# Kernel optimization log

Measured on AMD Instinct MI355X. Metric: run time of the kernel, lower is better.

## Reference

```python
import jax, jax.numpy as jnp
import numpy as np
from jax import lax

DILS = (1, 2, 4, 8)
POOLS = (1, 2, 3, 6)
EPS = 1e-3  # Keras BatchNormalization default epsilon


def conv2d(x, w, b, dil=1):
    y = lax.conv_general_dilated(x, w, window_strides=(1, 1), padding='SAME',
                                 rhs_dilation=(dil, dil),
                                 dimension_numbers=('NHWC', 'HWIO', 'NHWC'))
    return y + b


def bn(x, g, be, m, v):
    return (x - m) * (g * lax.rsqrt(v + EPS)) + be


def avg_pool_same(x, ps):
    if ps == 1:
        return x
    win = (1, ps, ps, 1)
    s = lax.reduce_window(x, 0.0, lax.add, win, win, 'SAME')
    c = lax.reduce_window(jnp.ones(x.shape[:3] + (1,), x.dtype), 0.0, lax.add, win, win, 'SAME')
    return s / c  # TF avg-pool SAME excludes padded zeros from the count


def setup_inputs() -> dict:
    key = jax.random.key(0)
    ks = iter(jax.random.split(key, 40))
    f = 64  # filters
    cin = 64
    d = {}
    d['x'] = jax.random.normal(next(ks), (2, 64, 64, cin), jnp.float32)
    nb = len(DILS)
    d['conv_w'] = jax.random.normal(next(ks), (nb, 3, 3, cin, f)) * 0.05
    d['conv_b'] = jax.random.normal(next(ks), (nb, f)) * 0.05
    d['bn_g'] = jnp.ones((nb, f)) + jax.random.normal(next(ks), (nb, f)) * 0.05
    d['bn_b'] = jax.random.normal(next(ks), (nb, f)) * 0.05
    d['bn_m'] = jax.random.normal(next(ks), (nb, f)) * 0.05
    d['bn_v'] = jax.random.uniform(next(ks), (nb, f), minval=0.5, maxval=1.5)
    dk = f // 8
    d['q_w'] = jax.random.normal(next(ks), (nb, 1, 1, f, dk)) * 0.05
    d['q_b'] = jax.random.normal(next(ks), (nb, dk)) * 0.05
    d['k_w'] = jax.random.normal(next(ks), (nb, 1, 1, f, dk)) * 0.05
    d['k_b'] = jax.random.normal(next(ks), (nb, dk)) * 0.05
    d['v_w'] = jax.random.normal(next(ks), (nb, 1, 1, f, f)) * 0.05
    d['v_b'] = jax.random.normal(next(ks), (nb, f)) * 0.05
    d['attn_gamma'] = jax.random.normal(next(ks), (nb,)) * 0.1
    cat = f * nb  # 256, input channels to pyramid convs
    npool = len(POOLS)
    fq = f // 4  # 16
    d['ppl_w'] = jax.random.normal(next(ks), (npool, 1, 1, cat, fq)) * 0.05
    d['ppl_b'] = jax.random.normal(next(ks), (npool, fq)) * 0.05
    d['ppl_bn_g'] = jnp.ones((npool, fq)) + jax.random.normal(next(ks), (npool, fq)) * 0.05
    d['ppl_bn_b'] = jax.random.normal(next(ks), (npool, fq)) * 0.05
    d['ppl_bn_m'] = jax.random.normal(next(ks), (npool, fq)) * 0.05
    d['ppl_bn_v'] = jax.random.uniform(next(ks), (npool, fq), minval=0.5, maxval=1.5)
    cfused = cat + npool * fq  # 320
    d['proj_w'] = jax.random.normal(next(ks), (1, 1, cfused, f)) * 0.05
    d['proj_b'] = jax.random.normal(next(ks), (f,)) * 0.05
    d['pbn_g'] = jnp.ones((f,)) + jax.random.normal(next(ks), (f,)) * 0.05
    d['pbn_b'] = jax.random.normal(next(ks), (f,)) * 0.05
    d['pbn_m'] = jax.random.normal(next(ks), (f,)) * 0.05
    d['pbn_v'] = jax.random.uniform(next(ks), (f,), minval=0.5, maxval=1.5)
    return d


def reference(x, conv_w, conv_b, bn_g, bn_b, bn_m, bn_v,
              q_w, q_b, k_w, k_b, v_w, v_b, attn_gamma,
              ppl_w, ppl_b, ppl_bn_g, ppl_bn_b, ppl_bn_m, ppl_bn_v,
              proj_w, proj_b, pbn_g, pbn_b, pbn_m, pbn_v):
    B, H, W, _ = x.shape
    branches = []
    for i, dil in enumerate(DILS):
        # dilated conv -> BN (inference) -> ReLU
        b = jax.nn.relu(bn(conv2d(x, conv_w[i], conv_b[i], dil),
                           bn_g[i], bn_b[i], bn_m[i], bn_v[i]))
        C = b.shape[-1]
        # full spatial self-attention over HW tokens
        q = conv2d(b, q_w[i], q_b[i]).reshape(B, H * W, -1)  # [B, HW, C/8]
        k = conv2d(b, k_w[i], k_b[i]).reshape(B, H * W, -1)
        v = conv2d(b, v_w[i], v_b[i]).reshape(B, H * W, C)
        attn = jax.nn.softmax(jnp.einsum('bnd,bmd->bnm', q, k), axis=-1)  # [B, HW, HW]
        o = jnp.einsum('bnm,bmc->bnc', attn, v).reshape(B, H, W, C)
        branches.append(attn_gamma[i] * o + b)
    fused = jnp.concatenate(branches, axis=-1)  # [B, H, W, 256]
    pooled = [fused]
    for j, ps in enumerate(POOLS):
        p = avg_pool_same(fused, ps)
        p = bn(conv2d(p, ppl_w[j], ppl_b[j]),
               ppl_bn_g[j], ppl_bn_b[j], ppl_bn_m[j], ppl_bn_v[j])
        p = jax.image.resize(p, (B, H, W, p.shape[-1]), method='bilinear')
        pooled.append(p)
    fused = jnp.concatenate(pooled, axis=-1)  # [B, H, W, 320]
    out = jax.nn.relu(bn(conv2d(fused, proj_w, proj_b), pbn_g, pbn_b, pbn_m, pbn_v))
    return out
```

## Files before the change

### kernel.cpp

```cpp
#include <hip/hip_runtime.h>
#include <hip/hip_bf16.h>
#include <stdint.h>

typedef unsigned short u16;
typedef short bs8 __attribute__((ext_vector_type(8)));
typedef unsigned short u16x4 __attribute__((ext_vector_type(4)));
typedef float vf4 __attribute__((ext_vector_type(4)));
typedef float vf16 __attribute__((ext_vector_type(16)));

__device__ __forceinline__ u16 f2bf(float f) {
    uint32_t u = __builtin_bit_cast(uint32_t, f);
    uint32_t r = u + 0x7FFFu + ((u >> 16) & 1u);
    return (u16)(r >> 16);
}
__device__ __forceinline__ float bf2f(u16 v) {
    return __builtin_bit_cast(float, (uint32_t)v << 16);
}

#define EPSBN 1e-3f
#define L2E 1.4426950408889634f

__global__ __launch_bounds__(256) void prep_k(
    const float* __restrict__ x, const float* __restrict__ cw,
    const float* __restrict__ qw, const float* __restrict__ kw,
    const float* __restrict__ vw, const float* __restrict__ pjw,
    u16* __restrict__ xbf, u16* __restrict__ wpk,
    u16* __restrict__ wqk_pk, u16* __restrict__ wv_pk, u16* __restrict__ wfin_pk)
{
    if (blockIdx.x < 512) {
        int t = blockIdx.x * 256 + threadIdx.x;
        int idx = t * 4;
        vf4 v = *(const vf4*)(x + idx);
        u16x4 o = { f2bf(v[0]), f2bf(v[1]), f2bf(v[2]), f2bf(v[3]) };
        *(u16x4*)(xbf + idx) = o;
    } else if (blockIdx.x < 1088) {
        int t2 = (blockIdx.x - 512) * 256 + threadIdx.x;
        if (t2 < 147456) {
            int cout = t2 & 63, rest = t2 >> 6;
            int cin = rest & 63, itap = rest >> 6;
            wpk[(((size_t)itap * 8 + (cin >> 3)) * 64 + cout) * 8 + (cin & 7)] = f2bf(cw[t2]);
        }
    } else if (blockIdx.x < 1168) {
        int t3 = (blockIdx.x - 1088) * 256 + threadIdx.x;
        if (t3 < 4096) {
            int j = t3 & 7, l = (t3 >> 3) & 63, kk = (t3 >> 9) & 1, i = t3 >> 10;
            int cin = kk * 32 + ((l >> 4) << 3) + j, row = l & 15;
            float val = (row < 8) ? qw[((size_t)(i * 64 + cin)) * 8 + row] * L2E
                                  : kw[((size_t)(i * 64 + cin)) * 8 + row - 8];
            wqk_pk[t3] = f2bf(val);
        } else {
            int e = t3 - 4096;
            int j = e & 7, l = (e >> 3) & 63, kk = (e >> 9) & 1;
            int ct = (e >> 10) & 3, i = e >> 12;
            int cin = kk * 32 + ((l >> 4) << 3) + j, cout = ct * 16 + (l & 15);
            wv_pk[e] = f2bf(vw[((size_t)(i * 64 + cin)) * 64 + cout]);
        }
    } else {
        int t4 = (blockIdx.x - 1168) * 256 + threadIdx.x;
        if (t4 < 20480) {
            int e = t4;
            int j = e & 7; e >>= 3;
            int rcol = e & 15; e >>= 4;
            int ct = e & 3; e >>= 2;
            int g = e & 3; int kc = e >> 2;
            int cin = kc * 32 + g * 8 + j, co = ct * 16 + rcol;
            wfin_pk[t4] = f2bf(pjw[(size_t)cin * 64 + co]);
        }
    }
}

__global__ __launch_bounds__(256) void conv_mfma_k(
    const u16* __restrict__ xbf, const u16* __restrict__ wpk,
    const float* __restrict__ cb, const float* __restrict__ bng,
    const float* __restrict__ bnb, const float* __restrict__ bnm,
    const float* __restrict__ bnv, const u16* __restrict__ wqk_pk,
    const u16* __restrict__ wv_pk, const float* __restrict__ qb,
    const float* __restrict__ kb, const float* __restrict__ vb,
    u16* __restrict__ b_bf, u16* __restrict__ qbuf,
    u16* __restrict__ kbuf, u16* __restrict__ vT)
{
    __shared__ u16 blds[32][72];
    const int ib = blockIdx.x & 7, pixtile = blockIdx.x >> 3;
    const int i = ib >> 1, b = ib & 1, dil = 1 << i;
    const int wave = __builtin_amdgcn_readfirstlane(threadIdx.x >> 6);
    const int lane = threadIdx.x & 63;
    const int g = lane >> 4, r = lane & 15;
    const int pixsub = wave & 1, ch = wave >> 1;
    const int pixbase = pixtile * 32 + pixsub * 16;
    const int h = pixbase >> 6, w0 = pixbase & 63;

    vf4 acc0 = {0.f, 0.f, 0.f, 0.f}, acc1 = {0.f, 0.f, 0.f, 0.f};

    for (int ky = 0; ky < 3; ++ky) {
        int hy = h + (ky - 1) * dil;
        if (hy < 0 || hy >= 64) continue;
        const u16* xrow = xbf + (size_t)((b * 64 + hy) * 64) * 64;
        for (int kx = 0; kx < 3; ++kx) {
            int wx = w0 + r + (kx - 1) * dil;
            bool valid = (wx >= 0) && (wx < 64);
            const u16* ap = xrow + (valid ? wx : 0) * 64 + g * 8;
            int tap = ky * 3 + kx;
            const u16* wb = wpk + (size_t)((i * 9 + tap) * 8) * 512;
#pragma unroll
            for (int c2 = 0; c2 < 2; ++c2) {
                bs8 av = {};
                if (valid) av = *(const bs8*)(ap + c2 * 32);
                const u16* bp = wb + (size_t)(c2 * 4 + g) * 512 + (ch * 32 + r) * 8;
                bs8 bv0 = *(const bs8*)(bp);
                bs8 bv1 = *(const bs8*)(bp + 16 * 8);
                acc0 = __builtin_amdgcn_mfma_f32_16x16x32_bf16(av, bv0, acc0, 0, 0, 0);
                acc1 = __builtin_amdgcn_mfma_f32_16x16x32_bf16(av, bv1, acc1, 0, 0, 0);
            }
        }
    }
#pragma unroll
    for (int ct = 0; ct < 2; ++ct) {
        int cidx = ch * 32 + ct * 16 + r;
        int cgl = i * 64 + cidx;
        float sc = bng[cgl] * rsqrtf(bnv[cgl] + EPSBN);
        float sh = (cb[cgl] - bnm[cgl]) * sc + bnb[cgl];
        vf4 a = ct ? acc1 : acc0;
#pragma unroll
        for (int rr = 0; rr < 4; ++rr) {
            float y = fmaxf(a[rr] * sc + sh, 0.f);
            u16 yb = f2bf(y);
            b_bf[((size_t)ib * 4096 + pixbase + g * 4 + rr) * 64 + cidx] = yb;
            blds[pixsub * 16 + g * 4 + rr][cidx] = yb;
        }
    }
    __syncthreads();

    const int ps2 = wave & 1, role = wave >> 1;
    const int n0 = pixtile * 32 + ps2 * 16;
    bs8 xb0 = *(const bs8*)(&blds[ps2 * 16 + r][g * 8]);
    bs8 xb1 = *(const bs8*)(&blds[ps2 * 16 + r][32 + g * 8]);

    if (role == 1) {
        const u16* wq = wqk_pk + (size_t)i * 1024 + lane * 8;
        bs8 wq0 = *(const bs8*)(wq);
        bs8 wq1 = *(const bs8*)(wq + 512);
        vf4 s = (vf4){0.f, 0.f, 0.f, 0.f};
        s = __builtin_amdgcn_mfma_f32_16x16x32_bf16(wq0, xb0, s, 0, 0, 0);
        s = __builtin_amdgcn_mfma_f32_16x16x32_bf16(wq1, xb1, s, 0, 0, 0);
        if (g < 2) {
            int d0 = g * 4;
            u16x4 o;
#pragma unroll
            for (int reg = 0; reg < 4; ++reg)
                o[reg] = f2bf(s[reg] + qb[i * 8 + d0 + reg] * L2E);
            *(u16x4*)(qbuf + ((size_t)ib * 4096 + n0 + r) * 8 + d0) = o;
        } else {
            int d0 = (g - 2) * 4;
            u16x4 o;
#pragma unroll
            for (int reg = 0; reg < 4; ++reg)
                o[reg] = f2bf(s[reg] + kb[i * 8 + d0 + reg]);
            *(u16x4*)(kbuf + ((size_t)ib * 4096 + n0 + r) * 8 + d0) = o;
        }
    }
#pragma unroll
    for (int c2t = 0; c2t < 2; ++c2t) {
        int ct = role * 2 + c2t;
        const u16* wv = wv_pk + ((size_t)i * 4 + ct) * 1024 + lane * 8;
        bs8 wv0 = *(const bs8*)(wv);
        bs8 wv1 = *(const bs8*)(wv + 512);
        vf4 a = (vf4){0.f, 0.f, 0.f, 0.f};
        a = __builtin_amdgcn_mfma_f32_16x16x32_bf16(wv0, xb0, a, 0, 0, 0);
        a = __builtin_amdgcn_mfma_f32_16x16x32_bf16(wv1, xb1, a, 0, 0, 0);
#pragma unroll
        for (int reg = 0; reg < 4; ++reg) {
            int row = ct * 16 + g * 4 + reg;
            vT[((size_t)ib * 64 + row) * 4096 + n0 + r] = f2bf(a[reg] + vb[i * 64 + row]);
        }
    }
}

__global__ __launch_bounds__(256) void attn_k(
    const u16* __restrict__ qbuf, const u16* __restrict__ kbuf,
    const u16* __restrict__ vT, u16* __restrict__ pacc,
    float* __restrict__ ppsum)
{
    __shared__ __align__(16) char smem[73728];

    const int bid = blockIdx.x;
    const int ib = bid & 7, ks = (bid >> 3) & 3, qblk = bid >> 5;
    const int yb = ks * 8 + ib;
    const int wave = __builtin_amdgcn_readfirstlane(threadIdx.x >> 6);
    const int lane = threadIdx.x & 63;
    const int ql = lane & 31;
    const int hb = lane >> 5;
    const int q0 = qblk * 256 + wave * 64;
    const int tid = threadIdx.x;

    const int kb_tbl[8] = {0, 8, 4, 12, 16, 24, 20, 28};
    const int kperm = (ql & 3) + kb_tbl[ql >> 2];

    bs8 qfa = {}, qfb = {};
    if (hb == 0) {
        qfa = *(const bs8*)(qbuf + ((size_t)ib * 4096 + q0 + ql) * 8);
        qfb = *(const bs8*)(qbuf + ((size_t)ib * 4096 + q0 + 32 + ql) * 8);
    }
    bs8 ones;
#pragma unroll
    for (int j = 0; j < 8; ++j) ones[j] = (short)0x3F80;

    vf16 a0a, a1a, a0b, a1b, sa, sb;
#pragma unroll
    for (int r = 0; r < 16; ++r) {
        a0a[r] = 0.f; a1a[r] = 0.f; a0b[r] = 0.f; a1b[r] = 0.f;
        sa[r] = 0.f; sb[r] = 0.f;
    }

    const u16* vsrc = vT + (size_t)ib * 64 * 4096;
    const u16* ksrc = kbuf + (size_t)ib * 4096 * 8;
    const int sc_ = tid >> 2, sp_ = tid & 3;

    bs8 vr[8]; bs8 kr;
    {
        const u16* vrow = vsrc + (size_t)sc_ * 4096 + (ks * 4) * 256;
#pragma unroll
        for (int s = 0; s < 8; ++s)
            vr[s] = *(const bs8*)(vrow + sp_ * 8 + s * 32);
        kr = *(const bs8*)(ksrc + (size_t)((ks * 4) * 256 + tid) * 8);
        char* ldsw = smem;
#pragma unroll
        for (int s = 0; s < 8; ++s) {
            int key = sp_ * 8 + s * 32;
            int lin = sc_ * 512 + key * 2;
            *(bs8*)(ldsw + (lin ^ ((sc_ & 7) << 4))) = vr[s];
        }
        *(bs8*)(ldsw + 32768 + tid * 16) = kr;
    }
    __syncthreads();

    for (int t = 0; t < 4; ++t) {
        if (t < 3) {
            const u16* vrow = vsrc + (size_t)sc_ * 4096 + (ks * 4 + t + 1) * 256;
#pragma unroll
            for (int s = 0; s < 8; ++s)
                vr[s] = *(const bs8*)(vrow + sp_ * 8 + s * 32);
            kr = *(const bs8*)(ksrc + (size_t)((ks * 4 + t + 1) * 256 + tid) * 8);
        }
        const char* ldsb = smem + (t & 1) * 36864;
        const u16* klds = (const u16*)(ldsb + 32768);

#pragma unroll 2
        for (int ck = 0; ck < 8; ++ck) {
            const int keyb = ck * 32;
            bs8 kA = {};
            if (hb == 0) kA = *(const bs8*)(klds + (keyb + kperm) * 8);
            vf16 z;
#pragma unroll
            for (int r = 0; r < 16; ++r) z[r] = 0.f;
            vf16 Sa = __builtin_amdgcn_mfma_f32_32x32x16_bf16(kA, qfa, z, 0, 0, 0);
            vf16 Sb = __builtin_amdgcn_mfma_f32_32x32x16_bf16(kA, qfb, z, 0, 0, 0);

            const int c0 = ql, c1 = 32 + ql;
            int lin00 = c0 * 512 + (keyb + hb * 8) * 2;
            int lin10 = c1 * 512 + (keyb + hb * 8) * 2;
            bs8 vA00 = *(const bs8*)(ldsb + (lin00 ^ ((c0 & 7) << 4)));
            bs8 vA01 = *(const bs8*)(ldsb + ((lin00 + 32) ^ ((c0 & 7) << 4)));
            bs8 vA10 = *(const bs8*)(ldsb + (lin10 ^ ((c1 & 7) << 4)));
            bs8 vA11 = *(const bs8*)(ldsb + ((lin10 + 32) ^ ((c1 & 7) << 4)));

            {
                float e[16];
#pragma unroll
                for (int r = 0; r < 16; ++r) e[r] = __builtin_amdgcn_exp2f(Sa[r]);
                union { uint32_t u[4]; bs8 v; } p0, p1;
#pragma unroll
                for (int j = 0; j < 4; ++j) {
                    uint32_t w0, w1;
                    asm("v_cvt_pk_bf16_f32 %0, %1, %2" : "=v"(w0) : "v"(e[2 * j]), "v"(e[2 * j + 1]));
                    asm("v_cvt_pk_bf16_f32 %0, %1, %2" : "=v"(w1) : "v"(e[8 + 2 * j]), "v"(e[8 + 2 * j + 1]));
                    p0.u[j] = w0;
                    p1.u[j] = w1;
                }
                sa = __builtin_amdgcn_mfma_f32_32x32x16_bf16(ones, p0.v, sa, 0, 0, 0);
                sa = __builtin_amdgcn_mfma_f32_32x32x16_bf16(ones, p1.v, sa, 0, 0, 0);
                a0a = __builtin_amdgcn_mfma_f32_32x32x16_bf16(vA00, p0.v, a0a, 0, 0, 0);
                a0a = __builtin_amdgcn_mfma_f32_32x32x16_bf16(vA01, p1.v, a0a, 0, 0, 0);
                a1a = __builtin_amdgcn_mfma_f32_32x32x16_bf16(vA10, p0.v, a1a, 0, 0, 0);
                a1a = __builtin_amdgcn_mfma_f32_32x32x16_bf16(vA11, p1.v, a1a, 0, 0, 0);
            }
            {
                float e[16];
#pragma unroll
                for (int r = 0; r < 16; ++r) e[r] = __builtin_amdgcn_exp2f(Sb[r]);
                union { uint32_t u[4]; bs8 v; } p0, p1;
#pragma unroll
                for (int j = 0; j < 4; ++j) {
                    uint32_t w0, w1;
                    asm("v_cvt_pk_bf16_f32 %0, %1, %2" : "=v"(w0) : "v"(e[2 * j]), "v"(e[2 * j + 1]));
                    asm("v_cvt_pk_bf16_f32 %0, %1, %2" : "=v"(w1) : "v"(e[8 + 2 * j]), "v"(e[8 + 2 * j + 1]));
                    p0.u[j] = w0;
                    p1.u[j] = w1;
                }
                sb = __builtin_amdgcn_mfma_f32_32x32x16_bf16(ones, p0.v, sb, 0, 0, 0);
                sb = __builtin_amdgcn_mfma_f32_32x32x16_bf16(ones, p1.v, sb, 0, 0, 0);
                a0b = __builtin_amdgcn_mfma_f32_32x32x16_bf16(vA00, p0.v, a0b, 0, 0, 0);
                a0b = __builtin_amdgcn_mfma_f32_32x32x16_bf16(vA01, p1.v, a0b, 0, 0, 0);
                a1b = __builtin_amdgcn_mfma_f32_32x32x16_bf16(vA10, p0.v, a1b, 0, 0, 0);
                a1b = __builtin_amdgcn_mfma_f32_32x32x16_bf16(vA11, p1.v, a1b, 0, 0, 0);
            }
        }

        if (t < 3) {
            char* ldsw = smem + ((t + 1) & 1) * 36864;
#pragma unroll
            for (int s = 0; s < 8; ++s) {
                int key = sp_ * 8 + s * 32;
                int lin = sc_ * 512 + key * 2;
                *(bs8*)(ldsw + (lin ^ ((sc_ & 7) << 4))) = vr[s];
            }
            *(bs8*)(ldsw + 32768 + tid * 16) = kr;
        }
        __syncthreads();
    }

    float* tw = (float*)smem + wave * 32 * 67;
#pragma unroll
    for (int t = 0; t < 2; ++t) {
        const int q0t = q0 + t * 32;
#pragma unroll
        for (int ct = 0; ct < 2; ++ct) {
            vf16 a = t ? (ct ? a1b : a0b) : (ct ? a1a : a0a);
#pragma unroll
            for (int r = 0; r < 16; ++r) {
                int c = ct * 32 + (r & 3) + 8 * (r >> 2) + 4 * hb;
                tw[ql * 67 + c] = a[r];
            }
        }
        __syncthreads();
        u16* pdst = pacc + ((size_t)yb * 4096 + q0t) * 64;
        for (int qq = 0; qq < 32; ++qq)
            pdst[(size_t)qq * 64 + lane] = f2bf(tw[qq * 67 + lane]);
        if (hb == 0)
            ppsum[(size_t)yb * 4096 + q0t + ql] = t ? sb[0] : sa[0];
    }
}

__global__ __launch_bounds__(256) void combine_k(
    const u16* __restrict__ pacc, const float* __restrict__ ppsum,
    const u16* __restrict__ b_bf, const float* __restrict__ gamma,
    u16* __restrict__ fusedbf)
{
    const int ib = blockIdx.x & 7, qb = blockIdx.x >> 3;
    const int i = ib >> 1, b = ib & 1;
    const int q = qb * 8 + (threadIdx.x >> 5);
    const int c2 = (threadIdx.x & 31) * 2;
    const size_t stride = (size_t)8 * 4096 * 64;
    size_t base = ((size_t)ib * 4096 + q) * 64 + c2;
    float lo = 0.f, hi = 0.f, ps = 0.f;
#pragma unroll
    for (int s = 0; s < 4; ++s) {
        uint32_t u = *(const uint32_t*)(pacc + base + s * stride);
        lo += bf2f((u16)(u & 0xffff));
        hi += bf2f((u16)(u >> 16));
        ps += ppsum[(size_t)(s * 8 + ib) * 4096 + q];
    }
    float rs = gamma[i] / ps;
    uint32_t bv = *(const uint32_t*)(b_bf + base);
    float o0 = rs * lo + bf2f((u16)(bv & 0xffff));
    float o1 = rs * hi + bf2f((u16)(bv >> 16));
    uint32_t ou = ((uint32_t)f2bf(o1) << 16) | f2bf(o0);
    *(uint32_t*)(fusedbf + ((size_t)b * 4096 + q) * 256 + i * 64 + c2) = ou;
}

__global__ __launch_bounds__(256) void pconv_k(
    const u16* __restrict__ fusedbf,
    const float* __restrict__ pw, const float* __restrict__ pbias,
    const float* __restrict__ pg, const float* __restrict__ pbe,
    const float* __restrict__ pm, const float* __restrict__ pv,
    float* __restrict__ po0, float* __restrict__ po1,
    float* __restrict__ po2, float* __restrict__ po3)
{
    __shared__ float plds[16][257];
    const int j = blockIdx.z, b = blockIdx.y;
    const int npix = (j == 0) ? 4096 : (j == 1) ? 1024 : (j == 2) ? 484 : 121;
    if (blockIdx.x * 16 >= npix) return;
    const int co = threadIdx.x & 15;
    const int pixl = threadIdx.x >> 4;
    const int pix = blockIdx.x * 16 + pixl;
    const float* wp = pw + (size_t)j * 256 * 16 + co;
    float acc = pbias[j * 16 + co];

    if (j == 0) {
        const u16* ip = fusedbf + ((size_t)b * 4096 + pix) * 256;
        for (int c8 = 0; c8 < 32; ++c8) {
            bs8 xv = *(const bs8*)(ip + c8 * 8);
#pragma unroll
            for (int e = 0; e < 8; ++e)
                acc = fmaf(bf2f((u16)xv[e]), wp[(c8 * 8 + e) * 16], acc);
        }
    } else {
        const int ps = (j == 1) ? 2 : (j == 2) ? 3 : 6;
        const int od = (j == 1) ? 32 : (j == 2) ? 22 : 11;
        if (pix < npix) {
            const int oh = pix / od, ow = pix % od;
            const int pad = (od * ps - 64) >> 1;
            int hs = oh * ps - pad, wss = ow * ps - pad;
            int h0 = max(hs, 0), h1 = min(hs + ps, 64);
            int w0 = max(wss, 0), w1 = min(wss + ps, 64);
            float s[16];
#pragma unroll
            for (int e = 0; e < 16; ++e) s[e] = 0.f;
            for (int hh = h0; hh < h1; ++hh)
                for (int ww = w0; ww < w1; ++ww) {
                    const u16* p = fusedbf + (((size_t)b * 4096) + hh * 64 + ww) * 256 + co * 16;
                    bs8 v0 = *(const bs8*)(p);
                    bs8 v1 = *(const bs8*)(p + 8);
#pragma unroll
                    for (int e = 0; e < 8; ++e) {
                        s[e] += bf2f((u16)v0[e]);
                        s[8 + e] += bf2f((u16)v1[e]);
                    }
                }
            float inv = 1.f / (float)((h1 - h0) * (w1 - w0));
#pragma unroll
            for (int e = 0; e < 16; ++e) plds[pixl][co * 16 + e] = s[e] * inv;
        }
        __syncthreads();
        if (pix < npix)
            for (int c = 0; c < 256; ++c)
                acc = fmaf(plds[pixl][c], wp[c * 16], acc);
    }
    if (pix < npix) {
        acc = (acc - pm[j * 16 + co]) * (pg[j * 16 + co] * rsqrtf(pv[j * 16 + co] + EPSBN)) + pbe[j * 16 + co];
        float* outp = (j == 0) ? po0 : (j == 1) ? po1 : (j == 2) ? po2 : po3;
        outp[((size_t)b * npix + pix) * 16 + co] = acc;
    }
}

__global__ __launch_bounds__(64) void final_gemm_k(
    const u16* __restrict__ fusedbf, const float* __restrict__ po0,
    const float* __restrict__ po1, const float* __restrict__ po2,
    const float* __restrict__ po3, const u16* __restrict__ wfin_pk,
    const float* __restrict__ pjb, const float* __restrict__ g,
    const float* __restrict__ be, const float* __restrict__ m,
    const float* __restrict__ v, float* __restrict__ out)
{
    const int gpix0 = blockIdx.x * 16;
    const int lane = threadIdx.x & 63;
    const int gg = lane >> 4, r = lane & 15;

    const int p = gpix0 + r;
    const int b = p >> 12, hw = p & 4095, h = hw >> 6, w = hw & 63;
    bs8 pav[2];
#pragma unroll
    for (int t = 0; t < 2; ++t) {
        int jj = t * 2 + (gg >> 1);
        int cc0 = (gg & 1) * 8;
        const float* P = (jj == 0) ? po0 : (jj == 1) ? po1 : (jj == 2) ? po2 : po3;
        int od = (jj == 0) ? 64 : (jj == 1) ? 32 : (jj == 2) ? 22 : 11;
        float scale = (float)od / 64.f;
        float fy = (h + 0.5f) * scale - 0.5f;
        int y0 = (int)floorf(fy);
        float ay = fy - (float)y0;
        int y1 = min(y0 + 1, od - 1);
        y0 = max(y0, 0);
        float fx = (w + 0.5f) * scale - 0.5f;
        int x0 = (int)floorf(fx);
        float ax = fx - (float)x0;
        int x1 = min(x0 + 1, od - 1);
        x0 = max(x0, 0);
        const float* B0 = P + (size_t)b * od * od * 16 + cc0;
        const float* p00 = B0 + (size_t)(y0 * od + x0) * 16;
        const float* p01 = B0 + (size_t)(y0 * od + x1) * 16;
        const float* p10 = B0 + (size_t)(y1 * od + x0) * 16;
        const float* p11 = B0 + (size_t)(y1 * od + x1) * 16;
        union { u16 s[8]; bs8 v8; } o;
#pragma unroll
        for (int cc = 0; cc < 8; ++cc) {
            float top = p00[cc] + ax * (p01[cc] - p00[cc]);
            float bot = p10[cc] + ax * (p11[cc] - p10[cc]);
            o.s[cc] = f2bf(top + ay * (bot - top));
        }
        pav[t] = o.v8;
    }

    vf4 acc[4];
#pragma unroll
    for (int ct = 0; ct < 4; ++ct) acc[ct] = (vf4){0.f, 0.f, 0.f, 0.f};

    const u16* fa = fusedbf + (size_t)p * 256 + gg * 8;
#pragma unroll
    for (int kc = 0; kc < 10; ++kc) {
        bs8 av = (kc < 8) ? *(const bs8*)(fa + kc * 32) : pav[kc - 8];
        const u16* wb = wfin_pk + (size_t)((kc * 4 + gg) * 4) * 128 + r * 8;
#pragma unroll
        for (int ct = 0; ct < 4; ++ct) {
            bs8 bv = *(const bs8*)(wb + ct * 128);
            acc[ct] = __builtin_amdgcn_mfma_f32_16x16x32_bf16(av, bv, acc[ct], 0, 0, 0);
        }
    }
#pragma unroll
    for (int ct = 0; ct < 4; ++ct) {
        int c = ct * 16 + r;
        float sc = g[c] * rsqrtf(v[c] + EPSBN);
        float sh = (pjb[c] - m[c]) * sc + be[c];
#pragma unroll
        for (int reg = 0; reg < 4; ++reg) {
            int pix = gpix0 + gg * 4 + reg;
            out[(size_t)pix * 64 + c] = fmaxf(acc[ct][reg] * sc + sh, 0.f);
        }
    }
}

extern "C" void kernel_launch(void* const* d_in, const int* in_sizes, int n_in,
                              void* d_out, int out_size, void* d_ws, size_t ws_size,
                              hipStream_t stream)
{
    const float* x      = (const float*)d_in[0];
    const float* conv_w = (const float*)d_in[1];
    const float* conv_b = (const float*)d_in[2];
    const float* bn_g   = (const float*)d_in[3];
    const float* bn_b   = (const float*)d_in[4];
    const float* bn_m   = (const float*)d_in[5];
    const float* bn_v   = (const float*)d_in[6];
    const float* q_w    = (const float*)d_in[7];
    const float* q_b    = (const float*)d_in[8];
    const float* k_w    = (const float*)d_in[9];
    const float* k_b    = (const float*)d_in[10];
    const float* v_w    = (const float*)d_in[11];
    const float* v_b    = (const float*)d_in[12];
    const float* gamma  = (const float*)d_in[13];
    const float* ppl_w  = (const float*)d_in[14];
    const float* ppl_b  = (const float*)d_in[15];
    const float* ppl_g  = (const float*)d_in[16];
    const float* ppl_be = (const float*)d_in[17];
    const float* ppl_m  = (const float*)d_in[18];
    const float* ppl_v  = (const float*)d_in[19];
    const float* proj_w = (const float*)d_in[20];
    const float* proj_b = (const float*)d_in[21];
    const float* pbn_g  = (const float*)d_in[22];
    const float* pbn_b  = (const float*)d_in[23];
    const float* pbn_m  = (const float*)d_in[24];
    const float* pbn_v  = (const float*)d_in[25];

    char* ws = (char*)d_ws;
    u16*  xbf     = (u16*)(ws + 0);
    u16*  wpk     = (u16*)(ws + 1048576);
    u16*  wqk_pk  = (u16*)(ws + 1343488);
    u16*  wv_pk   = (u16*)(ws + 1351680);
    u16*  wfin_pk = (u16*)(ws + 1384448);
    u16*  b_bf    = (u16*)(ws + 1425408);
    u16*  qbuf    = (u16*)(ws + 5619712);
    u16*  kbuf    = (u16*)(ws + 6144000);
    u16*  vT      = (u16*)(ws + 6668288);
    u16*  fusedbf = (u16*)(ws + 10862592);
    float* ppsum  = (float*)(ws + 15056896);
    u16*  pacc    = (u16*)(ws + 15581184);
    float* po0    = (float*)(ws + 18917376);
    float* po1    = (float*)(ws + 19441664);
    float* po2    = (float*)(ws + 19572736);
    float* po3    = (float*)(ws + 19634688);
    float* out    = (float*)d_out;

    prep_k<<<dim3(1248), 256, 0, stream>>>(
        x, conv_w, q_w, k_w, v_w, proj_w, xbf, wpk, wqk_pk, wv_pk, wfin_pk);
    conv_mfma_k<<<dim3(1024), 256, 0, stream>>>(
        xbf, wpk, conv_b, bn_g, bn_b, bn_m, bn_v,
        wqk_pk, wv_pk, q_b, k_b, v_b, b_bf, qbuf, kbuf, vT);
    attn_k<<<dim3(512), 256, 0, stream>>>(qbuf, kbuf, vT, pacc, ppsum);
    combine_k<<<dim3(4096), 256, 0, stream>>>(pacc, ppsum, b_bf, gamma, fusedbf);
    pconv_k<<<dim3(256, 2, 4), 256, 0, stream>>>(
        fusedbf, ppl_w, ppl_b, ppl_g, ppl_be, ppl_m, ppl_v,
        po0, po1, po2, po3);
    final_gemm_k<<<dim3(512), 64, 0, stream>>>(
        fusedbf, po0, po1, po2, po3, wfin_pk, proj_b, pbn_g, pbn_b, pbn_m, pbn_v, out);
}
```

Measured before the change: 102.3 us.

## Split attention keys eight ways with single-buffered LDS and VALU row sums

The attention kernel now splits the keys into 8 chunks instead of 4, doubling the grid to 1024 blocks, and combine_k sums eight partials. LDS use is halved by dropping the double-buffered register prefetch in favour of a synchronous load-then-compute loop, which should let more blocks fit per CU. The softmax denominator is accumulated with VALU adds plus a cross-half shuffle instead of extra MFMAs against a ones matrix, and s_setprio is placed around the MFMA groups. In exchange, global loads no longer overlap compute, and the partial-sum buffers move and double in size, which may strain the workspace and add traffic in combine_k.

```diff
diff --git a/kernel.cpp b/kernel.cpp
--- a/kernel.cpp
+++ b/kernel.cpp
@@ -180,10 +180,11 @@
     const u16* __restrict__ vT, u16* __restrict__ pacc,
     float* __restrict__ ppsum)
 {
-    __shared__ __align__(16) char smem[73728];
+    __shared__ __align__(16) char smem[36864];
+    u16* klds = (u16*)(smem + 32768);
 
     const int bid = blockIdx.x;
-    const int ib = bid & 7, ks = (bid >> 3) & 3, qblk = bid >> 5;
+    const int ib = bid & 7, ks = (bid >> 3) & 7, qblk = bid >> 6;
     const int yb = ks * 8 + ib;
     const int wave = __builtin_amdgcn_readfirstlane(threadIdx.x >> 6);
     const int lane = threadIdx.x & 63;
@@ -200,49 +201,34 @@
         qfa = *(const bs8*)(qbuf + ((size_t)ib * 4096 + q0 + ql) * 8);
         qfb = *(const bs8*)(qbuf + ((size_t)ib * 4096 + q0 + 32 + ql) * 8);
     }
-    bs8 ones;
-#pragma unroll
-    for (int j = 0; j < 8; ++j) ones[j] = (short)0x3F80;
-
-    vf16 a0a, a1a, a0b, a1b, sa, sb;
-#pragma unroll
-    for (int r = 0; r < 16; ++r) {
-        a0a[r] = 0.f; a1a[r] = 0.f; a0b[r] = 0.f; a1b[r] = 0.f;
-        sa[r] = 0.f; sb[r] = 0.f;
-    }
+
+    vf16 a0a, a1a, a0b, a1b;
+#pragma unroll
+    for (int r = 0; r < 16; ++r) { a0a[r] = 0.f; a1a[r] = 0.f; a0b[r] = 0.f; a1b[r] = 0.f; }
+    float psa = 0.f, psb = 0.f;
 
     const u16* vsrc = vT + (size_t)ib * 64 * 4096;
     const u16* ksrc = kbuf + (size_t)ib * 4096 * 8;
     const int sc_ = tid >> 2, sp_ = tid & 3;
-
-    bs8 vr[8]; bs8 kr;
-    {
-        const u16* vrow = vsrc + (size_t)sc_ * 4096 + (ks * 4) * 256;
-#pragma unroll
-        for (int s = 0; s < 8; ++s)
-            vr[s] = *(const bs8*)(vrow + sp_ * 8 + s * 32);
-        kr = *(const bs8*)(ksrc + (size_t)((ks * 4) * 256 + tid) * 8);
-        char* ldsw = smem;
-#pragma unroll
-        for (int s = 0; s < 8; ++s) {
-            int key = sp_ * 8 + s * 32;
-            int lin = sc_ * 512 + key * 2;
-            *(bs8*)(ldsw + (lin ^ ((sc_ & 7) << 4))) = vr[s];
-        }
-        *(bs8*)(ldsw + 32768 + tid * 16) = kr;
-    }
-    __syncthreads();
-
-    for (int t = 0; t < 4; ++t) {
-        if (t < 3) {
-            const u16* vrow = vsrc + (size_t)sc_ * 4096 + (ks * 4 + t + 1) * 256;
-#pragma unroll
-            for (int s = 0; s < 8; ++s)
-                vr[s] = *(const bs8*)(vrow + sp_ * 8 + s * 32);
-            kr = *(const bs8*)(ksrc + (size_t)((ks * 4 + t + 1) * 256 + tid) * 8);
-        }
-        const char* ldsb = smem + (t & 1) * 36864;
-        const u16* klds = (const u16*)(ldsb + 32768);
+    const char* ldsb = (const char*)smem;
+
+    for (int kblk = ks * 2; kblk < ks * 2 + 2; ++kblk) {
+        const int kb = kblk * 256;
+        __syncthreads();
+        {
+            const u16* vrow = vsrc + (size_t)sc_ * 4096 + kb;
+            char* ldsw = (char*)smem;
+#pragma unroll
+            for (int s = 0; s < 8; ++s) {
+                int key = sp_ * 8 + s * 32;
+                bs8 val = *(const bs8*)(vrow + key);
+                int lin = sc_ * 512 + key * 2;
+                *(bs8*)(ldsw + (lin ^ ((sc_ & 7) << 4))) = val;
+            }
+            bs8 kvv = *(const bs8*)(ksrc + (size_t)(kb + tid) * 8);
+            *(bs8*)(klds + tid * 8) = kvv;
+        }
+        __syncthreads();
 
 #pragma unroll 2
         for (int ck = 0; ck < 8; ++ck) {
@@ -252,8 +238,10 @@
             vf16 z;
 #pragma unroll
             for (int r = 0; r < 16; ++r) z[r] = 0.f;
+            __builtin_amdgcn_s_setprio(1);
             vf16 Sa = __builtin_amdgcn_mfma_f32_32x32x16_bf16(kA, qfa, z, 0, 0, 0);
             vf16 Sb = __builtin_amdgcn_mfma_f32_32x32x16_bf16(kA, qfb, z, 0, 0, 0);
+            __builtin_amdgcn_s_setprio(0);
 
             const int c0 = ql, c1 = 32 + ql;
             int lin00 = c0 * 512 + (keyb + hb * 8) * 2;
@@ -266,7 +254,10 @@
             {
                 float e[16];
 #pragma unroll
-                for (int r = 0; r < 16; ++r) e[r] = __builtin_amdgcn_exp2f(Sa[r]);
+                for (int r = 0; r < 16; ++r) {
+                    e[r] = __builtin_amdgcn_exp2f(Sa[r]);
+                    psa += e[r];
+                }
                 union { uint32_t u[4]; bs8 v; } p0, p1;
 #pragma unroll
                 for (int j = 0; j < 4; ++j) {
@@ -276,17 +267,20 @@
                     p0.u[j] = w0;
                     p1.u[j] = w1;
                 }
-                sa = __builtin_amdgcn_mfma_f32_32x32x16_bf16(ones, p0.v, sa, 0, 0, 0);
-                sa = __builtin_amdgcn_mfma_f32_32x32x16_bf16(ones, p1.v, sa, 0, 0, 0);
+                __builtin_amdgcn_s_setprio(1);
                 a0a = __builtin_amdgcn_mfma_f32_32x32x16_bf16(vA00, p0.v, a0a, 0, 0, 0);
                 a0a = __builtin_amdgcn_mfma_f32_32x32x16_bf16(vA01, p1.v, a0a, 0, 0, 0);
                 a1a = __builtin_amdgcn_mfma_f32_32x32x16_bf16(vA10, p0.v, a1a, 0, 0, 0);
                 a1a = __builtin_amdgcn_mfma_f32_32x32x16_bf16(vA11, p1.v, a1a, 0, 0, 0);
+                __builtin_amdgcn_s_setprio(0);
             }
             {
                 float e[16];
 #pragma unroll
-                for (int r = 0; r < 16; ++r) e[r] = __builtin_amdgcn_exp2f(Sb[r]);
+                for (int r = 0; r < 16; ++r) {
+                    e[r] = __builtin_amdgcn_exp2f(Sb[r]);
+                    psb += e[r];
+                }
                 union { uint32_t u[4]; bs8 v; } p0, p1;
 #pragma unroll
                 for (int j = 0; j < 4; ++j) {
@@ -296,28 +290,20 @@
                     p0.u[j] = w0;
                     p1.u[j] = w1;
                 }
-                sb = __builtin_amdgcn_mfma_f32_32x32x16_bf16(ones, p0.v, sb, 0, 0, 0);
-                sb = __builtin_amdgcn_mfma_f32_32x32x16_bf16(ones, p1.v, sb, 0, 0, 0);
+                __builtin_amdgcn_s_setprio(1);
                 a0b = __builtin_amdgcn_mfma_f32_32x32x16_bf16(vA00, p0.v, a0b, 0, 0, 0);
                 a0b = __builtin_amdgcn_mfma_f32_32x32x16_bf16(vA01, p1.v, a0b, 0, 0, 0);
                 a1b = __builtin_amdgcn_mfma_f32_32x32x16_bf16(vA10, p0.v, a1b, 0, 0, 0);
                 a1b = __builtin_amdgcn_mfma_f32_32x32x16_bf16(vA11, p1.v, a1b, 0, 0, 0);
+                __builtin_amdgcn_s_setprio(0);
             }
         }
-
-        if (t < 3) {
-            char* ldsw = smem + ((t + 1) & 1) * 36864;
-#pragma unroll
-            for (int s = 0; s < 8; ++s) {
-                int key = sp_ * 8 + s * 32;
-                int lin = sc_ * 512 + key * 2;
-                *(bs8*)(ldsw + (lin ^ ((sc_ & 7) << 4))) = vr[s];
-            }
-            *(bs8*)(ldsw + 32768 + tid * 16) = kr;
-        }
-        __syncthreads();
-    }
-
+    }
+
+    psa += __shfl_xor(psa, 32);
+    psb += __shfl_xor(psb, 32);
+
+    __syncthreads();
     float* tw = (float*)smem + wave * 32 * 67;
 #pragma unroll
     for (int t = 0; t < 2; ++t) {
@@ -331,12 +317,11 @@
                 tw[ql * 67 + c] = a[r];
             }
         }
-        __syncthreads();
         u16* pdst = pacc + ((size_t)yb * 4096 + q0t) * 64;
         for (int qq = 0; qq < 32; ++qq)
             pdst[(size_t)qq * 64 + lane] = f2bf(tw[qq * 67 + lane]);
         if (hb == 0)
-            ppsum[(size_t)yb * 4096 + q0t + ql] = t ? sb[0] : sa[0];
+            ppsum[(size_t)yb * 4096 + q0t + ql] = t ? psb : psa;
     }
 }
 
@@ -353,7 +338,7 @@
     size_t base = ((size_t)ib * 4096 + q) * 64 + c2;
     float lo = 0.f, hi = 0.f, ps = 0.f;
 #pragma unroll
-    for (int s = 0; s < 4; ++s) {
+    for (int s = 0; s < 8; ++s) {
         uint32_t u = *(const uint32_t*)(pacc + base + s * stride);
         lo += bf2f((u16)(u & 0xffff));
         hi += bf2f((u16)(u >> 16));
@@ -550,7 +535,7 @@
     u16*  vT      = (u16*)(ws + 6668288);
     u16*  fusedbf = (u16*)(ws + 10862592);
     float* ppsum  = (float*)(ws + 15056896);
-    u16*  pacc    = (u16*)(ws + 15581184);
+    u16*  pacc    = (u16*)(ws + 16105472);
     float* po0    = (float*)(ws + 18917376);
     float* po1    = (float*)(ws + 19441664);
     float* po2    = (float*)(ws + 19572736);
@@ -562,7 +547,7 @@
     conv_mfma_k<<<dim3(1024), 256, 0, stream>>>(
         xbf, wpk, conv_b, bn_g, bn_b, bn_m, bn_v,
         wqk_pk, wv_pk, q_b, k_b, v_b, b_bf, qbuf, kbuf, vT);
-    attn_k<<<dim3(512), 256, 0, stream>>>(qbuf, kbuf, vT, pacc, ppsum);
+    attn_k<<<dim3(1024), 256, 0, stream>>>(qbuf, kbuf, vT, pacc, ppsum);
     combine_k<<<dim3(4096), 256, 0, stream>>>(pacc, ppsum, b_bf, gamma, fusedbf);
     pconv_k<<<dim3(256, 2, 4), 256, 0, stream>>>(
         fusedbf, ppl_w, ppl_b, ppl_g, ppl_be, ppl_m, ppl_v,
```

After: 100.9 us. Within noise of the previous version (-1.4%).
